# Kernel optimization log

Measured on AMD Instinct MI355X. Metric: run time of the kernel, lower is better.

The kernel has to match this reference:

```python
import jax, jax.numpy as jnp
import numpy as np
import math

DIM = 384; HEADS = 12; HD = 32; L_REL = 4; L_STD = 12; MLP_H = 4 * DIM
B = 8; N = 256
N_REL = 1
TIME_SCALE = 30000.0 / 500 * 0.3
SCALE = HD ** -0.5
NEG = -1e9  # finite stand-in for -inf padding mask (identical softmax result, safe grads)


def _ln(x, g, b):
    m = x.mean(-1, keepdims=True)
    v = ((x - m) ** 2).mean(-1, keepdims=True)
    return (x - m) / jnp.sqrt(v + 1e-5) * g + b


def _sin_emb(x, dim):
    half = dim // 2
    freq = jnp.exp(jnp.arange(half, dtype=x.dtype) * (-math.log(10000.0) / half))
    e = x[..., None] * freq
    return jnp.concatenate([jnp.sin(e), jnp.cos(e)], -1)


def _rel_bias(x0, w1d, b1d, wp, bp):
    pos = x0[..., :3]
    t = x0[..., 3:4]
    dpos = pos[:, :, None] - pos[:, None, :]                 # [B,N,N,3]
    dt = t[:, :, None] - t[:, None, :] * TIME_SCALE          # [B,N,N,1] (scale on 2nd term, as in torch)
    dpos2 = dpos ** 2
    dt2 = dt ** 2
    ds2 = dpos2.sum(-1) - dt2[..., 0]
    d = jnp.sign(ds2) * jnp.sqrt(jnp.abs(ds2))
    f = jnp.concatenate([dpos, dt, dpos2, dt2], -1)          # [B,N,N,8]
    d = d + (f @ w1d.T + b1d)[..., 0]
    emb = _sin_emb(1024.0 * jnp.clip(d, -4.0, 4.0), HD)      # [B,N,N,HD]
    return emb @ wp.T + bp


def _mask_bias(mask):
    mn = jnp.minimum(mask[:, None, :], mask[:, :, None])
    mx = jnp.maximum(mask[:, None, :], mask[:, :, None])
    return jnp.where(mx < 0, 0.0, mn)                        # [B,N,N]


def _attn(xq, xkv, wq, wk, wv, wo, bo, rel, mbias):
    Bq, Nq, _ = xq.shape
    q = (xq @ wq.T).reshape(Bq, Nq, HEADS, HD).transpose(0, 2, 1, 3) * SCALE
    k = (xkv @ wk.T).reshape(Bq, Nq, HEADS, HD).transpose(0, 2, 1, 3)
    v = (xkv @ wv.T).reshape(Bq, Nq, HEADS, HD).transpose(0, 2, 1, 3)
    a = jnp.einsum('bhic,bhjc->bhij', q, k)
    if rel is not None:
        a = a + jnp.einsum('bhic,bijc->bhij', q, rel)
    if mbias is not None:
        a = a + mbias[:, None]
    a = jax.nn.softmax(a, axis=-1)
    o = jnp.einsum('bhij,bhjc->bihc', a, v)
    if rel is not None:
        o = o + jnp.einsum('bhij,bijc->bihc', a, rel)
    return o.reshape(Bq, Nq, HEADS * HD) @ wo.T + bo


def _mlp(x, w1, b1, w2, b2):
    return jax.nn.gelu(x @ w1.T + b1, approximate=False) @ w2.T + b2


def setup_inputs() -> dict:
    key = jax.random.key(0)
    ks = iter(jax.random.split(key, 64))
    f = lambda shape: jax.random.normal(next(ks), shape, jnp.float32) * 0.02
    inp = {}
    inp['x'] = jax.random.normal(next(ks), (B, N, DIM), jnp.float32)
    inp['x0'] = jax.random.normal(next(ks), (B, N, 4), jnp.float32)
    lengths = jax.random.randint(next(ks), (B,), N // 2, N + 1)
    inp['mask'] = jnp.where(jnp.arange(N)[None, :] < lengths[:, None], 0.0, NEG).astype(jnp.float32)
    inp['rp_w1d'] = f((1, 8)); inp['rp_b1d'] = jnp.zeros((1,), jnp.float32)
    inp['rp_wp'] = f((HD, HD)); inp['rp_bp'] = jnp.zeros((HD,), jnp.float32)
    for p, L in (('sw', L_REL), ('bl', L_STD)):
        inp[p + '_ln1_g'] = jnp.ones((L, DIM), jnp.float32); inp[p + '_ln1_b'] = jnp.zeros((L, DIM), jnp.float32)
        inp[p + '_ln2_g'] = jnp.ones((L, DIM), jnp.float32); inp[p + '_ln2_b'] = jnp.zeros((L, DIM), jnp.float32)
        inp[p + '_wq'] = f((L, DIM, DIM)); inp[p + '_wk'] = f((L, DIM, DIM)); inp[p + '_wv'] = f((L, DIM, DIM))
        inp[p + '_wo'] = f((L, DIM, DIM)); inp[p + '_bo'] = jnp.zeros((L, DIM), jnp.float32)
        inp[p + '_w1'] = f((L, MLP_H, DIM)); inp[p + '_b1'] = jnp.zeros((L, MLP_H), jnp.float32)
        inp[p + '_w2'] = f((L, DIM, MLP_H)); inp[p + '_b2'] = jnp.zeros((L, DIM), jnp.float32)
    inp['bl_g1'] = jnp.ones((L_STD, DIM), jnp.float32)   # init_values=1
    inp['bl_g2'] = jnp.ones((L_STD, DIM), jnp.float32)
    inp['cls_w'] = f((DIM,))
    inp['out_w'] = f((3, DIM)); inp['out_b'] = jnp.zeros((3,), jnp.float32)
    return inp


def reference(x, x0, mask, rp_w1d, rp_b1d, rp_wp, rp_bp,
              sw_ln1_g, sw_ln1_b, sw_ln2_g, sw_ln2_b, sw_wq, sw_wk, sw_wv, sw_wo, sw_bo,
              sw_w1, sw_b1, sw_w2, sw_b2,
              bl_ln1_g, bl_ln1_b, bl_ln2_g, bl_ln2_b, bl_wq, bl_wk, bl_wv, bl_wo, bl_bo,
              bl_w1, bl_b1, bl_w2, bl_b2, bl_g1, bl_g2, cls_w, out_w, out_b):
    rel = _rel_bias(x0, rp_w1d, rp_b1d, rp_wp, rp_bp)
    mbias = _mask_bias(mask)
    for i in range(L_REL):
        r = rel if i < N_REL else None
        xn = _ln(x, sw_ln1_g[i], sw_ln1_b[i])
        x = x + _attn(xn, xn, sw_wq[i], sw_wk[i], sw_wv[i], sw_wo[i], sw_bo[i], r, mbias)
        x = x + _mlp(_ln(x, sw_ln2_g[i], sw_ln2_b[i]), sw_w1[i], sw_b1[i], sw_w2[i], sw_b2[i])
    # prepend cls token; it is always valid
    cls = jnp.broadcast_to(cls_w[None, None, :], (x.shape[0], 1, DIM))
    x = jnp.concatenate([cls, x], axis=1)
    mask2 = jnp.concatenate([jnp.zeros((x.shape[0], 1), mask.dtype), mask], axis=1)
    mbias2 = _mask_bias(mask2)
    for i in range(L_STD):
        xn = _ln(x, bl_ln1_g[i], bl_ln1_b[i])
        x = x + bl_g1[i] * _attn(xn, xn, bl_wq[i], bl_wk[i], bl_wv[i], bl_wo[i], bl_bo[i], None, mbias2)
        x = x + bl_g2[i] * _mlp(_ln(x, bl_ln2_g[i], bl_ln2_b[i]), bl_w1[i], bl_b1[i], bl_w2[i], bl_b2[i])
    return x[:, 0] @ out_w.T + out_b   # [B, 3]
```

## Files before the change

### kernel.cpp

```cpp
#include <hip/hip_runtime.h>
#include <hip/hip_bf16.h>
#include <math.h>

#define DIM 384
#define HEADS 12
#define HD 32
#define MLP_H 1536
#define BATCH 8
#define N1 256
#define N2 257
#define QP 1152
#define SCALE 0.17677669529663687f
#define TIME_SCALE 18.0f

typedef __attribute__((ext_vector_type(8))) short frag8;
typedef __attribute__((ext_vector_type(4))) float f32x4;

__device__ inline short f2bf(float x) {
    __hip_bfloat16 h = __float2bfloat16(x);
    short s;
    __builtin_memcpy(&s, &h, 2);
    return s;
}
__device__ inline float bf2f(short s) {
    unsigned u = ((unsigned)(unsigned short)s) << 16;
    float f;
    __builtin_memcpy(&f, &u, 4);
    return f;
}

__global__ __launch_bounds__(256) void conv_kernel(
        const float* __restrict__ in, short* __restrict__ out, int n) {
    int i = (blockIdx.x * 256 + threadIdx.x) * 4;
    if (i >= n) return;
    float4 v = *(const float4*)(in + i);
    out[i]     = f2bf(v.x);
    out[i + 1] = f2bf(v.y);
    out[i + 2] = f2bf(v.z);
    out[i + 3] = f2bf(v.w);
}

__global__ __launch_bounds__(256) void conv_qkv_kernel(
        const float* __restrict__ wq, const float* __restrict__ wk,
        const float* __restrict__ wv, short* __restrict__ out, int L) {
    size_t idx = ((size_t)blockIdx.x * 256 + threadIdx.x) * 4;
    size_t total = (size_t)L * QP * DIM;
    if (idx >= total) return;
    size_t k = idx % DIM;
    size_t row = idx / DIM;
    size_t r = row % QP;
    size_t l = row / QP;
    int which = (int)(r / DIM);
    int rr = (int)(r % DIM);
    const float* src = ((which == 0) ? wq : (which == 1) ? wk : wv)
                     + (l * DIM + rr) * DIM + k;
    float4 v = *(const float4*)src;
    out[idx]     = f2bf(v.x);
    out[idx + 1] = f2bf(v.y);
    out[idx + 2] = f2bf(v.z);
    out[idx + 3] = f2bf(v.w);
}

__global__ __launch_bounds__(256) void rel_kernel(
        const float* __restrict__ x0, const float* __restrict__ w1d,
        const float* __restrict__ b1d, const float* __restrict__ wp,
        const float* __restrict__ bp, short* __restrict__ rel) {
    __shared__ float swp[HD * HD];
    __shared__ float sbp[HD];
    __shared__ float sw1[8];
    __shared__ float sb1;
    __shared__ float sfreq[16];
    int tid = threadIdx.x;
    for (int i = tid; i < HD * HD; i += 256) swp[i] = wp[i];
    if (tid < HD) sbp[tid] = bp[tid];
    if (tid < 8) sw1[tid] = w1d[tid];
    if (tid == 0) sb1 = b1d[0];
    if (tid < 16) sfreq[tid] = expf(-(float)tid * 0.5756462732485114f);
    __syncthreads();

    int gid = blockIdx.x * 256 + tid;
    int j  = gid & (N1 - 1);
    int bi = gid >> 8;
    int i  = bi & (N1 - 1);
    int b  = bi >> 8;

    const float* pi = x0 + (size_t)(b * N1 + i) * 4;
    const float* pj = x0 + (size_t)(b * N1 + j) * 4;
    float dx = pi[0] - pj[0], dy = pi[1] - pj[1], dz = pi[2] - pj[2];
    float dt = pi[3] - pj[3] * TIME_SCALE;
    float dx2 = dx * dx, dy2 = dy * dy, dz2 = dz * dz, dt2 = dt * dt;
    float ds2 = dx2 + dy2 + dz2 - dt2;
    float d = copysignf(sqrtf(fabsf(ds2)), ds2);
    d += dx * sw1[0] + dy * sw1[1] + dz * sw1[2] + dt * sw1[3]
       + dx2 * sw1[4] + dy2 * sw1[5] + dz2 * sw1[6] + dt2 * sw1[7] + sb1;
    d = fminf(fmaxf(d, -4.f), 4.f) * 1024.f;

    float emb[32];
    #pragma unroll
    for (int k = 0; k < 16; k++) {
        float s, c;
        sincosf(d * sfreq[k], &s, &c);
        emb[k] = s; emb[16 + k] = c;
    }
    short* out = rel + (size_t)gid * HD;
    #pragma unroll 4
    for (int c = 0; c < HD; c++) {
        float a = sbp[c];
        #pragma unroll
        for (int k = 0; k < 32; k++) a += emb[k] * swp[c * 32 + k];
        out[c] = f2bf(a);
    }
}

__global__ __launch_bounds__(128) void ln_kernel(
        const float* __restrict__ x, const float* __restrict__ g,
        const float* __restrict__ b, short* __restrict__ y) {
    int r = blockIdx.x;
    int t = threadIdx.x;
    const float* xr = x + (size_t)r * DIM;
    float v0 = xr[t], v1 = xr[t + 128], v2 = xr[t + 256];
    __shared__ float redm[2], redv[2];
    float s = v0 + v1 + v2;
    for (int o = 32; o; o >>= 1) s += __shfl_down(s, o, 64);
    int lane = t & 63, wid = t >> 6;
    if (!lane) redm[wid] = s;
    __syncthreads();
    float mean = (redm[0] + redm[1]) * (1.f / DIM);
    float d0 = v0 - mean, d1 = v1 - mean, d2 = v2 - mean;
    float s2 = d0 * d0 + d1 * d1 + d2 * d2;
    for (int o = 32; o; o >>= 1) s2 += __shfl_down(s2, o, 64);
    if (!lane) redv[wid] = s2;
    __syncthreads();
    float var = (redv[0] + redv[1]) * (1.f / DIM);
    float rs = rsqrtf(var + 1e-5f);
    short* yr = y + (size_t)r * DIM;
    yr[t]       = f2bf(d0 * rs * g[t]       + b[t]);
    yr[t + 128] = f2bf(d1 * rs * g[t + 128] + b[t + 128]);
    yr[t + 256] = f2bf(d2 * rs * g[t + 256] + b[t + 256]);
}

__global__ __launch_bounds__(512) void gemm_bf16_kernel(
        const short* __restrict__ A, const short* __restrict__ W,
        const float* __restrict__ bias, const float* __restrict__ resid,
        const float* __restrict__ gvec, float* __restrict__ Cf,
        short* __restrict__ Cb, int M, int Np, int K, int mode) {
    __shared__ short As2[2][2][4][64][8];
    __shared__ short Bs2[2][2][4][64][8];
    int tid = threadIdx.x;
    int w = tid >> 6, lane = tid & 63;
    int nlo = lane & 15, quad = lane >> 4;
    int g = w >> 2, wl = w & 3;
    int wm = wl >> 1, wn = wl & 1;
    int n0 = blockIdx.x * 64, m0 = blockIdx.y * 64;

    f32x4 acc00 = {0.f, 0.f, 0.f, 0.f}, acc01 = {0.f, 0.f, 0.f, 0.f};
    f32x4 acc10 = {0.f, 0.f, 0.f, 0.f}, acc11 = {0.f, 0.f, 0.f, 0.f};

    int oct16 = tid & 15, rbase = tid >> 4;
    int kh_s = oct16 >> 3, oo = oct16 & 7, ks_s = oo >> 2, q_s = oo & 3;
    const frag8 fz = {0, 0, 0, 0, 0, 0, 0, 0};
    frag8 pa0 = fz, pa1 = fz, pb0, pb1;

    {
        int gm0 = m0 + rbase, gm1 = m0 + rbase + 32;
        if (gm0 < M) pa0 = *(const frag8*)(A + (size_t)gm0 * K + oct16 * 8);
        if (gm1 < M) pa1 = *(const frag8*)(A + (size_t)gm1 * K + oct16 * 8);
        pb0 = *(const frag8*)(W + (size_t)(n0 + rbase) * K + oct16 * 8);
        pb1 = *(const frag8*)(W + (size_t)(n0 + rbase + 32) * K + oct16 * 8);
    }

    for (int k0 = 0; k0 < K; k0 += 128) {
        *(frag8*)&As2[kh_s][ks_s][q_s][rbase][0]      = pa0;
        *(frag8*)&As2[kh_s][ks_s][q_s][rbase + 32][0] = pa1;
        *(frag8*)&Bs2[kh_s][ks_s][q_s][rbase][0]      = pb0;
        *(frag8*)&Bs2[kh_s][ks_s][q_s][rbase + 32][0] = pb1;
        __syncthreads();
        int kn = k0 + 128;
        if (kn < K) {
            int gm0 = m0 + rbase, gm1 = m0 + rbase + 32;
            pa0 = fz; pa1 = fz;
            if (gm0 < M) pa0 = *(const frag8*)(A + (size_t)gm0 * K + kn + oct16 * 8);
            if (gm1 < M) pa1 = *(const frag8*)(A + (size_t)gm1 * K + kn + oct16 * 8);
            pb0 = *(const frag8*)(W + (size_t)(n0 + rbase) * K + kn + oct16 * 8);
            pb1 = *(const frag8*)(W + (size_t)(n0 + rbase + 32) * K + kn + oct16 * 8);
        }
        #pragma unroll
        for (int ks = 0; ks < 2; ks++) {
            frag8 a0 = *(const frag8*)&As2[g][ks][quad][wm * 32 + nlo][0];
            frag8 a1 = *(const frag8*)&As2[g][ks][quad][wm * 32 + 16 + nlo][0];
            frag8 b0 = *(const frag8*)&Bs2[g][ks][quad][wn * 32 + nlo][0];
            frag8 b1 = *(const frag8*)&Bs2[g][ks][quad][wn * 32 + 16 + nlo][0];
            acc00 = __builtin_amdgcn_mfma_f32_16x16x32_bf16(a0, b0, acc00, 0, 0, 0);
            acc01 = __builtin_amdgcn_mfma_f32_16x16x32_bf16(a0, b1, acc01, 0, 0, 0);
            acc10 = __builtin_amdgcn_mfma_f32_16x16x32_bf16(a1, b0, acc10, 0, 0, 0);
            acc11 = __builtin_amdgcn_mfma_f32_16x16x32_bf16(a1, b1, acc11, 0, 0, 0);
        }
        __syncthreads();
    }

    f32x4* red4 = (f32x4*)&As2[0][0][0][0][0];
    int roff = wl * 64 + lane;
    if (g == 1) {
        red4[roff]       = acc00;
        red4[256 + roff] = acc01;
        red4[512 + roff] = acc10;
        red4[768 + roff] = acc11;
    }
    __syncthreads();
    if (g == 1) return;
    {
        f32x4 t0 = red4[roff], t1 = red4[256 + roff];
        f32x4 t2 = red4[512 + roff], t3 = red4[768 + roff];
        #pragma unroll
        for (int r = 0; r < 4; r++) {
            acc00[r] += t0[r]; acc01[r] += t1[r];
            acc10[r] += t2[r]; acc11[r] += t3[r];
        }
    }

    #pragma unroll
    for (int mi = 0; mi < 2; mi++) {
        #pragma unroll
        for (int nf = 0; nf < 2; nf++) {
            f32x4 av = (mi == 0) ? ((nf == 0) ? acc00 : acc01)
                                 : ((nf == 0) ? acc10 : acc11);
            int col = n0 + wn * 32 + nf * 16 + nlo;
            float bcol = (mode >= 1) ? bias[col] : 0.f;
            float gs = 1.f;
            if (mode == 2 && gvec) gs = gvec[col];
            #pragma unroll
            for (int r = 0; r < 4; r++) {
                int row = m0 + wm * 32 + mi * 16 + quad * 4 + r;
                if (row >= M) continue;
                float v = av[r] + bcol;
                if (mode == 1) v = 0.5f * v * (1.f + erff(v * 0.70710678118654752f));
                if (mode == 2) {
                    Cf[(size_t)row * Np + col] = resid[(size_t)row * Np + col] + gs * v;
                } else {
                    Cb[(size_t)row * Np + col] = f2bf(v);
                }
            }
        }
    }
}

__global__ __launch_bounds__(256) void attn_mfma_kernel(
        const short* __restrict__ qkv, const float* __restrict__ maskv,
        short* __restrict__ ob, int Nseq) {
    __shared__ short kf[18][64][8];
    __shared__ short vf[9][2][64][8];
    __shared__ short pbuf[4][16][40];
    __shared__ float ms[320];

    int tid = threadIdx.x;
    int w = tid >> 6, lane = tid & 63;
    int n = lane & 15, quad = lane >> 4;
    int qg = blockIdx.x, h = blockIdx.y, b = blockIdx.z;
    size_t rowB = (size_t)(b * Nseq);

    for (int j = tid; j < 320; j += 256)
        ms[j] = (j < Nseq) ? maskv[b * Nseq + j] : 0.f;

    {
        int c0 = (tid & 3) * 8;
        for (int j = tid >> 2; j < 288; j += 64) {
            frag8 kk = {0, 0, 0, 0, 0, 0, 0, 0};
            frag8 vv = {0, 0, 0, 0, 0, 0, 0, 0};
            if (j < Nseq) {
                const short* base = qkv + (rowB + j) * QP + h * HD + c0;
                kk = *(const frag8*)(base + 384);
                vv = *(const frag8*)(base + 768);
            }
            *(frag8*)&kf[j >> 4][(c0 >> 3) * 16 + (j & 15)][0] = kk;
            #pragma unroll
            for (int e = 0; e < 8; e++) {
                int c = c0 + e;
                vf[j >> 5][c >> 4][((j & 31) >> 3) * 16 + (c & 15)][j & 7] = vv[e];
            }
        }
    }

    int i0 = qg * 64 + w * 16;
    frag8 qa = {0, 0, 0, 0, 0, 0, 0, 0};
    {
        int i = i0 + n;
        if (i < Nseq) qa = *(const frag8*)(qkv + (rowB + i) * QP + h * HD + quad * 8);
    }
    __syncthreads();

    float msq[4];
    #pragma unroll
    for (int r = 0; r < 4; r++) msq[r] = ms[i0 + quad * 4 + r];

    float mrow[4], lsum[4];
    #pragma unroll
    for (int r = 0; r < 4; r++) { mrow[r] = -3.0e38f; lsum[r] = 0.f; }
    f32x4 oacc0 = {0.f, 0.f, 0.f, 0.f}, oacc1 = {0.f, 0.f, 0.f, 0.f};

    for (int jb = 0; jb < 9; jb++) {
        frag8 kb0 = *(const frag8*)&kf[2 * jb][lane][0];
        frag8 kb1 = *(const frag8*)&kf[2 * jb + 1][lane][0];
        f32x4 z = {0.f, 0.f, 0.f, 0.f};
        f32x4 s0 = __builtin_amdgcn_mfma_f32_16x16x32_bf16(qa, kb0, z, 0, 0, 0);
        f32x4 s1 = __builtin_amdgcn_mfma_f32_16x16x32_bf16(qa, kb1, z, 0, 0, 0);

        int j0 = jb * 32 + n;
        int j1 = j0 + 16;
        float mj0 = ms[j0], mj1 = ms[j1];
        float pad0 = (j0 < Nseq) ? 0.f : -1e9f;
        float pad1 = (j1 < Nseq) ? 0.f : -1e9f;

        #pragma unroll
        for (int r = 0; r < 4; r++) {
            float mi = msq[r];
            float b0 = ((fmaxf(mi, mj0) < 0.f) ? 0.f : fminf(mi, mj0)) + pad0;
            float b1 = ((fmaxf(mi, mj1) < 0.f) ? 0.f : fminf(mi, mj1)) + pad1;
            float v0 = s0[r] * SCALE + b0;
            float v1 = s1[r] * SCALE + b1;
            float rm = fmaxf(v0, v1);
            rm = fmaxf(rm, __shfl_xor(rm, 1));
            rm = fmaxf(rm, __shfl_xor(rm, 2));
            rm = fmaxf(rm, __shfl_xor(rm, 4));
            rm = fmaxf(rm, __shfl_xor(rm, 8));
            float mn = fmaxf(mrow[r], rm);
            float alpha = __expf(mrow[r] - mn);
            mrow[r] = mn;
            float p0 = __expf(v0 - mn);
            float p1 = __expf(v1 - mn);
            float ps = p0 + p1;
            ps += __shfl_xor(ps, 1);
            ps += __shfl_xor(ps, 2);
            ps += __shfl_xor(ps, 4);
            ps += __shfl_xor(ps, 8);
            lsum[r] = lsum[r] * alpha + ps;
            oacc0[r] *= alpha;
            oacc1[r] *= alpha;
            pbuf[w][quad * 4 + r][n]      = f2bf(p0);
            pbuf[w][quad * 4 + r][n + 16] = f2bf(p1);
        }
        __syncthreads();
        frag8 pa = *(const frag8*)&pbuf[w][n][quad * 8];
        frag8 vb0 = *(const frag8*)&vf[jb][0][lane][0];
        frag8 vb1 = *(const frag8*)&vf[jb][1][lane][0];
        oacc0 = __builtin_amdgcn_mfma_f32_16x16x32_bf16(pa, vb0, oacc0, 0, 0, 0);
        oacc1 = __builtin_amdgcn_mfma_f32_16x16x32_bf16(pa, vb1, oacc1, 0, 0, 0);
        __syncthreads();
    }

    #pragma unroll
    for (int r = 0; r < 4; r++) {
        int i = i0 + quad * 4 + r;
        if (i < Nseq) {
            float invl = 1.f / lsum[r];
            ob[(rowB + i) * DIM + h * HD + n]      = f2bf(oacc0[r] * invl);
            ob[(rowB + i) * DIM + h * HD + 16 + n] = f2bf(oacc1[r] * invl);
        }
    }
}

__global__ __launch_bounds__(256) void attn_rel_mfma_kernel(
        const short* __restrict__ qkv, const short* __restrict__ relb,
        const float* __restrict__ maskv, short* __restrict__ ob) {
    const int Nseq = N1;
    __shared__ short kf[16][64][8];
    __shared__ short vf[8][2][64][8];
    __shared__ short pbuf[4][16][40];
    __shared__ float qrow[4][16][32];
    __shared__ float orel[4][16][33];
    __shared__ float alphas[4][16];
    __shared__ float ms[256];

    int tid = threadIdx.x;
    int w = tid >> 6, lane = tid & 63;
    int n = lane & 15, quad = lane >> 4;
    int qg = blockIdx.x, h = blockIdx.y, b = blockIdx.z;
    size_t rowB = (size_t)(b * Nseq);

    if (tid < 256) ms[tid] = maskv[b * Nseq + tid];

    {
        int c0 = (tid & 3) * 8;
        for (int j = tid >> 2; j < 256; j += 64) {
            const short* base = qkv + (rowB + j) * QP + h * HD + c0;
            frag8 kk = *(const frag8*)(base + 384);
            frag8 vv = *(const frag8*)(base + 768);
            *(frag8*)&kf[j >> 4][(c0 >> 3) * 16 + (j & 15)][0] = kk;
            #pragma unroll
            for (int e = 0; e < 8; e++) {
                int c = c0 + e;
                vf[j >> 5][c >> 4][((j & 31) >> 3) * 16 + (c & 15)][j & 7] = vv[e];
            }
        }
    }

    int i0 = qg * 64 + w * 16;
    frag8 qa = *(const frag8*)(qkv + (rowB + i0 + n) * QP + h * HD + quad * 8);
    {
        int il = lane >> 2, c8 = (lane & 3) * 8;
        frag8 qv = *(const frag8*)(qkv + (rowB + i0 + il) * QP + h * HD + c8);
        #pragma unroll
        for (int e = 0; e < 8; e++) qrow[w][il][c8 + e] = bf2f(qv[e]) * SCALE;
    }
    __syncthreads();

    float msq[4];
    #pragma unroll
    for (int r = 0; r < 4; r++) msq[r] = ms[i0 + quad * 4 + r];

    float mrow[4], lsum[4];
    #pragma unroll
    for (int r = 0; r < 4; r++) { mrow[r] = -3.0e38f; lsum[r] = 0.f; }
    f32x4 oacc0 = {0.f, 0.f, 0.f, 0.f}, oacc1 = {0.f, 0.f, 0.f, 0.f};
    float arel[8];
    #pragma unroll
    for (int e = 0; e < 8; e++) arel[e] = 0.f;

    int il = lane & 15, oct = lane >> 4;
    const short* relrow = relb + (((size_t)b * N1 + (i0 + il)) * N1) * HD + oct * 8;

    for (int jb = 0; jb < 8; jb++) {
        frag8 kb0 = *(const frag8*)&kf[2 * jb][lane][0];
        frag8 kb1 = *(const frag8*)&kf[2 * jb + 1][lane][0];
        f32x4 z = {0.f, 0.f, 0.f, 0.f};
        f32x4 s0 = __builtin_amdgcn_mfma_f32_16x16x32_bf16(qa, kb0, z, 0, 0, 0);
        f32x4 s1 = __builtin_amdgcn_mfma_f32_16x16x32_bf16(qa, kb1, z, 0, 0, 0);

        int j0 = jb * 32 + n;
        int j1 = j0 + 16;
        float mj0 = ms[j0], mj1 = ms[j1];

        #pragma unroll
        for (int r = 0; r < 4; r++) {
            int i = i0 + quad * 4 + r;
            const short* r0 = relb + (((size_t)b * N1 + i) * N1 + j0) * HD;
            const short* r1 = relb + (((size_t)b * N1 + i) * N1 + j1) * HD;
            float d0 = 0.f, d1 = 0.f;
            #pragma unroll
            for (int c8 = 0; c8 < 4; c8++) {
                frag8 ra = *(const frag8*)(r0 + c8 * 8);
                frag8 rb_ = *(const frag8*)(r1 + c8 * 8);
                const float* qp = &qrow[w][quad * 4 + r][c8 * 8];
                #pragma unroll
                for (int e = 0; e < 8; e++) {
                    float qv = qp[e];
                    d0 += qv * bf2f(ra[e]);
                    d1 += qv * bf2f(rb_[e]);
                }
            }
            float mi = msq[r];
            float b0 = (fmaxf(mi, mj0) < 0.f) ? 0.f : fminf(mi, mj0);
            float b1 = (fmaxf(mi, mj1) < 0.f) ? 0.f : fminf(mi, mj1);
            float v0 = s0[r] * SCALE + d0 + b0;
            float v1 = s1[r] * SCALE + d1 + b1;
            float rm = fmaxf(v0, v1);
            rm = fmaxf(rm, __shfl_xor(rm, 1));
            rm = fmaxf(rm, __shfl_xor(rm, 2));
            rm = fmaxf(rm, __shfl_xor(rm, 4));
            rm = fmaxf(rm, __shfl_xor(rm, 8));
            float mn = fmaxf(mrow[r], rm);
            float alpha = __expf(mrow[r] - mn);
            mrow[r] = mn;
            float p0 = __expf(v0 - mn);
            float p1 = __expf(v1 - mn);
            float ps = p0 + p1;
            ps += __shfl_xor(ps, 1);
            ps += __shfl_xor(ps, 2);
            ps += __shfl_xor(ps, 4);
            ps += __shfl_xor(ps, 8);
            lsum[r] = lsum[r] * alpha + ps;
            oacc0[r] *= alpha;
            oacc1[r] *= alpha;
            pbuf[w][quad * 4 + r][n]      = f2bf(p0);
            pbuf[w][quad * 4 + r][n + 16] = f2bf(p1);
            if (n == 0) alphas[w][quad * 4 + r] = alpha;
        }
        __syncthreads();
        {
            float al = alphas[w][il];
            #pragma unroll
            for (int e = 0; e < 8; e++) arel[e] *= al;
            const short* rb2 = relrow + (size_t)(jb * 32) * HD;
            #pragma unroll 8
            for (int jj = 0; jj < 32; jj++) {
                float p = bf2f(pbuf[w][il][jj]);
                frag8 rv = *(const frag8*)(rb2 + (size_t)jj * HD);
                #pragma unroll
                for (int e = 0; e < 8; e++) arel[e] += p * bf2f(rv[e]);
            }
        }
        frag8 pa = *(const frag8*)&pbuf[w][n][quad * 8];
        frag8 vb0 = *(const frag8*)&vf[jb][0][lane][0];
        frag8 vb1 = *(const frag8*)&vf[jb][1][lane][0];
        oacc0 = __builtin_amdgcn_mfma_f32_16x16x32_bf16(pa, vb0, oacc0, 0, 0, 0);
        oacc1 = __builtin_amdgcn_mfma_f32_16x16x32_bf16(pa, vb1, oacc1, 0, 0, 0);
        __syncthreads();
    }

    #pragma unroll
    for (int e = 0; e < 8; e++) orel[w][il][oct * 8 + e] = arel[e];
    __syncthreads();

    #pragma unroll
    for (int r = 0; r < 4; r++) {
        int i = i0 + quad * 4 + r;
        float invl = 1.f / lsum[r];
        float o0 = (oacc0[r] + orel[w][quad * 4 + r][n])      * invl;
        float o1 = (oacc1[r] + orel[w][quad * 4 + r][16 + n]) * invl;
        ob[(rowB + i) * DIM + h * HD + n]      = f2bf(o0);
        ob[(rowB + i) * DIM + h * HD + 16 + n] = f2bf(o1);
    }
}

__global__ __launch_bounds__(256) void concat_kernel(
        const float* __restrict__ xa, const float* __restrict__ clsw,
        const float* __restrict__ mask, float* __restrict__ xb,
        float* __restrict__ m2) {
    int idx = blockIdx.x * 256 + threadIdx.x;
    const int total = BATCH * N2 * DIM;
    if (idx < total) {
        int c = idx % DIM;
        int tokb = idx / DIM;
        int p = tokb % N2, b = tokb / N2;
        xb[idx] = (p == 0) ? clsw[c] : xa[((size_t)(b * N1) + p - 1) * DIM + c];
    }
    if (idx < BATCH * N2) {
        int p = idx % N2, b = idx / N2;
        m2[idx] = (p == 0) ? 0.f : mask[b * N1 + p - 1];
    }
}

__global__ __launch_bounds__(64) void head_kernel(
        const float* __restrict__ xb, const float* __restrict__ ow,
        const float* __restrict__ obv, float* __restrict__ out) {
    int blk = blockIdx.x;
    int b = blk / 3, o = blk % 3;
    int lane = threadIdx.x;
    const float* xr = xb + (size_t)(b * N2) * DIM;
    const float* wr = ow + o * DIM;
    float s = 0.f;
    for (int c = lane; c < DIM; c += 64) s += xr[c] * wr[c];
    for (int off = 32; off; off >>= 1) s += __shfl_down(s, off, 64);
    if (!lane) out[blk] = s + obv[o];
}

extern "C" void kernel_launch(void* const* d_in, const int* in_sizes, int n_in,
                              void* d_out, int out_size, void* d_ws, size_t ws_size,
                              hipStream_t stream) {
    (void)in_sizes; (void)n_in; (void)out_size; (void)ws_size;
    const float* X       = (const float*)d_in[0];
    const float* X0      = (const float*)d_in[1];
    const float* MSK     = (const float*)d_in[2];
    const float* RW1     = (const float*)d_in[3];
    const float* RB1     = (const float*)d_in[4];
    const float* RWP     = (const float*)d_in[5];
    const float* RBP     = (const float*)d_in[6];
    const float* SW_LN1G = (const float*)d_in[7];
    const float* SW_LN1B = (const float*)d_in[8];
    const float* SW_LN2G = (const float*)d_in[9];
    const float* SW_LN2B = (const float*)d_in[10];
    const float* SW_WQ   = (const float*)d_in[11];
    const float* SW_WK   = (const float*)d_in[12];
    const float* SW_WV   = (const float*)d_in[13];
    const float* SW_WO   = (const float*)d_in[14];
    const float* SW_BO   = (const float*)d_in[15];
    const float* SW_W1   = (const float*)d_in[16];
    const float* SW_B1   = (const float*)d_in[17];
    const float* SW_W2   = (const float*)d_in[18];
    const float* SW_B2   = (const float*)d_in[19];
    const float* BL_LN1G = (const float*)d_in[20];
    const float* BL_LN1B = (const float*)d_in[21];
    const float* BL_LN2G = (const float*)d_in[22];
    const float* BL_LN2B = (const float*)d_in[23];
    const float* BL_WQ   = (const float*)d_in[24];
    const float* BL_WK   = (const float*)d_in[25];
    const float* BL_WV   = (const float*)d_in[26];
    const float* BL_WO   = (const float*)d_in[27];
    const float* BL_BO   = (const float*)d_in[28];
    const float* BL_W1   = (const float*)d_in[29];
    const float* BL_B1   = (const float*)d_in[30];
    const float* BL_W2   = (const float*)d_in[31];
    const float* BL_B2   = (const float*)d_in[32];
    const float* BL_G1   = (const float*)d_in[33];
    const float* BL_G2   = (const float*)d_in[34];
    const float* CLSW    = (const float*)d_in[35];
    const float* OUTW    = (const float*)d_in[36];
    const float* OUTB    = (const float*)d_in[37];

    const int T1 = BATCH * N1;
    const int T2 = BATCH * N2;
    const size_t RELSZ = (size_t)BATCH * N1 * N1 * HD;

    short* rel = (short*)d_ws;
    float* xa  = (float*)(rel + RELSZ);
    float* xb  = xa + (size_t)T1 * DIM;
    float* m2  = xb + (size_t)T2 * DIM;
    short* sbase = (short*)(m2 + 2064);
    short* xn   = sbase;
    short* qkv  = xn  + (size_t)T2 * DIM;
    short* ab   = qkv + (size_t)T2 * QP;
    short* hb   = ab  + (size_t)T2 * DIM;
    short* cw_qkv_sw = hb + (size_t)T2 * MLP_H;
    short* cw_qkv_bl = cw_qkv_sw + (size_t)4  * QP * DIM;
    short* cw_wo_sw  = cw_qkv_bl + (size_t)12 * QP * DIM;
    short* cw_wo_bl  = cw_wo_sw  + (size_t)4  * DIM * DIM;
    short* cw_w1_sw  = cw_wo_bl  + (size_t)12 * DIM * DIM;
    short* cw_w1_bl  = cw_w1_sw  + (size_t)4  * MLP_H * DIM;
    short* cw_w2_sw  = cw_w1_bl  + (size_t)12 * MLP_H * DIM;
    short* cw_w2_bl  = cw_w2_sw  + (size_t)4  * DIM * MLP_H;

    conv_qkv_kernel<<<(4 * QP * DIM / 4 + 255) / 256, 256, 0, stream>>>(SW_WQ, SW_WK, SW_WV, cw_qkv_sw, 4);
    conv_qkv_kernel<<<(12 * QP * DIM / 4 + 255) / 256, 256, 0, stream>>>(BL_WQ, BL_WK, BL_WV, cw_qkv_bl, 12);
    conv_kernel<<<(4 * DIM * DIM / 4 + 255) / 256, 256, 0, stream>>>(SW_WO, cw_wo_sw, 4 * DIM * DIM);
    conv_kernel<<<(12 * DIM * DIM / 4 + 255) / 256, 256, 0, stream>>>(BL_WO, cw_wo_bl, 12 * DIM * DIM);
    conv_kernel<<<(4 * MLP_H * DIM / 4 + 255) / 256, 256, 0, stream>>>(SW_W1, cw_w1_sw, 4 * MLP_H * DIM);
    conv_kernel<<<(12 * MLP_H * DIM / 4 + 255) / 256, 256, 0, stream>>>(BL_W1, cw_w1_bl, 12 * MLP_H * DIM);
    conv_kernel<<<(4 * DIM * MLP_H / 4 + 255) / 256, 256, 0, stream>>>(SW_W2, cw_w2_sw, 4 * DIM * MLP_H);
    conv_kernel<<<(12 * DIM * MLP_H / 4 + 255) / 256, 256, 0, stream>>>(BL_W2, cw_w2_bl, 12 * DIM * MLP_H);

    rel_kernel<<<BATCH * N1 * N1 / 256, 256, 0, stream>>>(X0, RW1, RB1, RWP, RBP, rel);
    hipMemcpyAsync(xa, X, sizeof(float) * T1 * DIM, hipMemcpyDeviceToDevice, stream);

    dim3 gQ1(QP / 64, T1 / 64);
    dim3 gP1(DIM / 64, T1 / 64);
    dim3 gM1(MLP_H / 64, T1 / 64);
    dim3 gF1(4, HEADS, BATCH);
    for (int l = 0; l < 4; l++) {
        const short* wqkv = cw_qkv_sw + (size_t)l * QP * DIM;
        const short* wo = cw_wo_sw + (size_t)l * DIM * DIM;
        const short* w1 = cw_w1_sw + (size_t)l * MLP_H * DIM;
        const short* w2 = cw_w2_sw + (size_t)l * DIM * MLP_H;
        const float* bo = SW_BO + (size_t)l * DIM;
        const float* b1 = SW_B1 + (size_t)l * MLP_H;
        const float* b2 = SW_B2 + (size_t)l * DIM;

        ln_kernel<<<T1, 128, 0, stream>>>(xa, SW_LN1G + l * DIM, SW_LN1B + l * DIM, xn);
        gemm_bf16_kernel<<<gQ1, 512, 0, stream>>>(xn, wqkv, nullptr, nullptr, nullptr,
                                                  nullptr, qkv, T1, QP, DIM, 0);
        if (l == 0)
            attn_rel_mfma_kernel<<<gF1, 256, 0, stream>>>(qkv, rel, MSK, ab);
        else
            attn_mfma_kernel<<<gF1, 256, 0, stream>>>(qkv, MSK, ab, N1);
        gemm_bf16_kernel<<<gP1, 512, 0, stream>>>(ab, wo, bo, xa, nullptr,
                                                  xa, nullptr, T1, DIM, DIM, 2);
        ln_kernel<<<T1, 128, 0, stream>>>(xa, SW_LN2G + l * DIM, SW_LN2B + l * DIM, xn);
        gemm_bf16_kernel<<<gM1, 512, 0, stream>>>(xn, w1, b1, nullptr, nullptr,
                                                  nullptr, hb, T1, MLP_H, DIM, 1);
        gemm_bf16_kernel<<<gP1, 512, 0, stream>>>(hb, w2, b2, xa, nullptr,
                                                  xa, nullptr, T1, DIM, MLP_H, 2);
    }

    concat_kernel<<<(BATCH * N2 * DIM + 255) / 256, 256, 0, stream>>>(xa, CLSW, MSK, xb, m2);

    int MB2 = (T2 + 63) / 64;
    dim3 gQ2(QP / 64, MB2);
    dim3 gP2(DIM / 64, MB2);
    dim3 gM2(MLP_H / 64, MB2);
    dim3 gF2(5, HEADS, BATCH);
    for (int l = 0; l < 12; l++) {
        const short* wqkv = cw_qkv_bl + (size_t)l * QP * DIM;
        const short* wo = cw_wo_bl + (size_t)l * DIM * DIM;
        const short* w1 = cw_w1_bl + (size_t)l * MLP_H * DIM;
        const short* w2 = cw_w2_bl + (size_t)l * DIM * MLP_H;
        const float* bo = BL_BO + (size_t)l * DIM;
        const float* b1 = BL_B1 + (size_t)l * MLP_H;
        const float* b2 = BL_B2 + (size_t)l * DIM;
        const float* g1 = BL_G1 + (size_t)l * DIM;
        const float* g2 = BL_G2 + (size_t)l * DIM;

        ln_kernel<<<T2, 128, 0, stream>>>(xb, BL_LN1G + l * DIM, BL_LN1B + l * DIM, xn);
        gemm_bf16_kernel<<<gQ2, 512, 0, stream>>>(xn, wqkv, nullptr, nullptr, nullptr,
                                                  nullptr, qkv, T2, QP, DIM, 0);
        attn_mfma_kernel<<<gF2, 256, 0, stream>>>(qkv, m2, ab, N2);
        gemm_bf16_kernel<<<gP2, 512, 0, stream>>>(ab, wo, bo, xb, g1,
                                                  xb, nullptr, T2, DIM, DIM, 2);
        ln_kernel<<<T2, 128, 0, stream>>>(xb, BL_LN2G + l * DIM, BL_LN2B + l * DIM, xn);
        gemm_bf16_kernel<<<gM2, 512, 0, stream>>>(xn, w1, b1, nullptr, nullptr,
                                                  nullptr, hb, T2, MLP_H, DIM, 1);
        gemm_bf16_kernel<<<gP2, 512, 0, stream>>>(hb, w2, b2, xb, g2,
                                                  xb, nullptr, T2, DIM, MLP_H, 2);
    }

    head_kernel<<<BATCH * 3, 64, 0, stream>>>(xb, OUTW, OUTB, (float*)d_out);
}
```

Baseline: 1.834 ms.

## Precompute rel-position scores with MFMA in a separate kernel for layer 0

Adds a rel_score_kernel that computes q·rel for all 12 heads of a query row with one MFMA per 16-key tile, so each rel row is read once and shared across heads. The result is written as a bf16 [B,H,N,N] buffer. The attention kernel then reads one precomputed scalar per (i,j) instead of re-reading rel and doing per-head scalar dot products. The attention kernel also moves to 128-thread blocks with twice as many blocks. The cost is an extra launch, an extra global buffer round-trip, and an additional bf16 rounding of the rel scores.

```diff
diff --git a/kernel.cpp b/kernel.cpp
--- a/kernel.cpp
+++ b/kernel.cpp
@@ -109,6 +109,37 @@
         #pragma unroll
         for (int k = 0; k < 32; k++) a += emb[k] * swp[c * 32 + k];
         out[c] = f2bf(a);
+    }
+}
+
+__global__ __launch_bounds__(256) void rel_score_kernel(
+        const short* __restrict__ qkv, const short* __restrict__ relb,
+        short* __restrict__ rs) {
+    int tid = threadIdx.x;
+    int w = tid >> 6, lane = tid & 63;
+    int n = lane & 15, quad = lane >> 4;
+    int i = blockIdx.x * 4 + w;
+    int b = blockIdx.y;
+
+    const frag8 fz = {0, 0, 0, 0, 0, 0, 0, 0};
+    frag8 qa = fz;
+    if (n < HEADS)
+        qa = *(const frag8*)(qkv + ((size_t)(b * N1) + i) * QP + n * HD + quad * 8);
+
+    const short* relrow = relb + (((size_t)(b * N1) + i) * N1) * HD;
+    const f32x4 z = {0.f, 0.f, 0.f, 0.f};
+
+    #pragma unroll 4
+    for (int jt = 0; jt < 16; jt++) {
+        frag8 rb = *(const frag8*)(relrow + (size_t)(jt * 16 + n) * HD + quad * 8);
+        f32x4 s = __builtin_amdgcn_mfma_f32_16x16x32_bf16(qa, rb, z, 0, 0, 0);
+        #pragma unroll
+        for (int r = 0; r < 4; r++) {
+            int h = quad * 4 + r;
+            if (h < HEADS)
+                rs[((size_t)(b * HEADS + h) * N1 + i) * N1 + jt * 16 + n] =
+                    f2bf(s[r] * SCALE);
+        }
     }
 }
 
@@ -358,16 +389,16 @@
     }
 }
 
-__global__ __launch_bounds__(256) void attn_rel_mfma_kernel(
+__global__ __launch_bounds__(128) void attn_rel_mfma_kernel(
         const short* __restrict__ qkv, const short* __restrict__ relb,
-        const float* __restrict__ maskv, short* __restrict__ ob) {
+        const short* __restrict__ rs, const float* __restrict__ maskv,
+        short* __restrict__ ob) {
     const int Nseq = N1;
     __shared__ short kf[16][64][8];
     __shared__ short vf[8][2][64][8];
-    __shared__ short pbuf[4][16][40];
-    __shared__ float qrow[4][16][32];
-    __shared__ float orel[4][16][33];
-    __shared__ float alphas[4][16];
+    __shared__ short pbuf[2][16][40];
+    __shared__ float orel[2][16][33];
+    __shared__ float alphas[2][16];
     __shared__ float ms[256];
 
     int tid = threadIdx.x;
@@ -376,11 +407,11 @@
     int qg = blockIdx.x, h = blockIdx.y, b = blockIdx.z;
     size_t rowB = (size_t)(b * Nseq);
 
-    if (tid < 256) ms[tid] = maskv[b * Nseq + tid];
+    for (int jj = tid; jj < 256; jj += 128) ms[jj] = maskv[b * Nseq + jj];
 
     {
         int c0 = (tid & 3) * 8;
-        for (int j = tid >> 2; j < 256; j += 64) {
+        for (int j = tid >> 2; j < 256; j += 32) {
             const short* base = qkv + (rowB + j) * QP + h * HD + c0;
             frag8 kk = *(const frag8*)(base + 384);
             frag8 vv = *(const frag8*)(base + 768);
@@ -393,19 +424,17 @@
         }
     }
 
-    int i0 = qg * 64 + w * 16;
+    int i0 = qg * 32 + w * 16;
     frag8 qa = *(const frag8*)(qkv + (rowB + i0 + n) * QP + h * HD + quad * 8);
-    {
-        int il = lane >> 2, c8 = (lane & 3) * 8;
-        frag8 qv = *(const frag8*)(qkv + (rowB + i0 + il) * QP + h * HD + c8);
-        #pragma unroll
-        for (int e = 0; e < 8; e++) qrow[w][il][c8 + e] = bf2f(qv[e]) * SCALE;
-    }
     __syncthreads();
 
     float msq[4];
-    #pragma unroll
-    for (int r = 0; r < 4; r++) msq[r] = ms[i0 + quad * 4 + r];
+    const short* rsp[4];
+    #pragma unroll
+    for (int r = 0; r < 4; r++) {
+        msq[r] = ms[i0 + quad * 4 + r];
+        rsp[r] = rs + ((size_t)(b * HEADS + h) * N1 + (i0 + quad * 4 + r)) * N1;
+    }
 
     float mrow[4], lsum[4];
     #pragma unroll
@@ -431,22 +460,8 @@
 
         #pragma unroll
         for (int r = 0; r < 4; r++) {
-            int i = i0 + quad * 4 + r;
-            const short* r0 = relb + (((size_t)b * N1 + i) * N1 + j0) * HD;
-            const short* r1 = relb + (((size_t)b * N1 + i) * N1 + j1) * HD;
-            float d0 = 0.f, d1 = 0.f;
-            #pragma unroll
-            for (int c8 = 0; c8 < 4; c8++) {
-                frag8 ra = *(const frag8*)(r0 + c8 * 8);
-                frag8 rb_ = *(const frag8*)(r1 + c8 * 8);
-                const float* qp = &qrow[w][quad * 4 + r][c8 * 8];
-                #pragma unroll
-                for (int e = 0; e < 8; e++) {
-                    float qv = qp[e];
-                    d0 += qv * bf2f(ra[e]);
-                    d1 += qv * bf2f(rb_[e]);
-                }
-            }
+            float d0 = bf2f(rsp[r][j0]);
+            float d1 = bf2f(rsp[r][j1]);
             float mi = msq[r];
             float b0 = (fmaxf(mi, mj0) < 0.f) ? 0.f : fminf(mi, mj0);
             float b1 = (fmaxf(mi, mj1) < 0.f) ? 0.f : fminf(mi, mj1);
@@ -607,6 +622,7 @@
     short* cw_w1_bl  = cw_w1_sw  + (size_t)4  * MLP_H * DIM;
     short* cw_w2_sw  = cw_w1_bl  + (size_t)12 * MLP_H * DIM;
     short* cw_w2_bl  = cw_w2_sw  + (size_t)4  * DIM * MLP_H;
+    short* rs_buf    = cw_w2_bl  + (size_t)12 * DIM * MLP_H;
 
     conv_qkv_kernel<<<(4 * QP * DIM / 4 + 255) / 256, 256, 0, stream>>>(SW_WQ, SW_WK, SW_WV, cw_qkv_sw, 4);
     conv_qkv_kernel<<<(12 * QP * DIM / 4 + 255) / 256, 256, 0, stream>>>(BL_WQ, BL_WK, BL_WV, cw_qkv_bl, 12);
@@ -624,6 +640,7 @@
     dim3 gP1(DIM / 64, T1 / 64);
     dim3 gM1(MLP_H / 64, T1 / 64);
     dim3 gF1(4, HEADS, BATCH);
+    dim3 gRel(8, HEADS, BATCH);
     for (int l = 0; l < 4; l++) {
         const short* wqkv = cw_qkv_sw + (size_t)l * QP * DIM;
         const short* wo = cw_wo_sw + (size_t)l * DIM * DIM;
@@ -636,10 +653,12 @@
         ln_kernel<<<T1, 128, 0, stream>>>(xa, SW_LN1G + l * DIM, SW_LN1B + l * DIM, xn);
         gemm_bf16_kernel<<<gQ1, 512, 0, stream>>>(xn, wqkv, nullptr, nullptr, nullptr,
                                                   nullptr, qkv, T1, QP, DIM, 0);
-        if (l == 0)
-            attn_rel_mfma_kernel<<<gF1, 256, 0, stream>>>(qkv, rel, MSK, ab);
-        else
+        if (l == 0) {
+            rel_score_kernel<<<dim3(N1 / 4, BATCH), 256, 0, stream>>>(qkv, rel, rs_buf);
+            attn_rel_mfma_kernel<<<gRel, 128, 0, stream>>>(qkv, rel, rs_buf, MSK, ab);
+        } else {
             attn_mfma_kernel<<<gF1, 256, 0, stream>>>(qkv, MSK, ab, N1);
+        }
         gemm_bf16_kernel<<<gP1, 512, 0, stream>>>(ab, wo, bo, xa, nullptr,
                                                   xa, nullptr, T1, DIM, DIM, 2);
         ln_kernel<<<T1, 128, 0, stream>>>(xa, SW_LN2G + l * DIM, SW_LN2B + l * DIM, xn);
```

After: 1.811 ms. Within noise of the previous version (-1.3%).
